# Kernel tuning notes

Hardware: AMD Instinct MI355X
Metric: run time of the kernel (lower is better)

The kernel has to match this reference:

```python
import jax, jax.numpy as jnp
import numpy as np

NUM_HEADS = 16
KERNEL_SIZE = 13  # odd, neighborhood size nh = 6


def setup_inputs() -> dict:
    key = jax.random.key(0)
    ks = jax.random.split(key, 6)
    B, L, C = 4, 4096, 512
    return {
        "x": jax.random.normal(ks[0], (B, L, C), dtype=jnp.float32),
        "qkv_w": jax.random.normal(ks[1], (3 * C, C), dtype=jnp.float32) * (C ** -0.5),
        "qkv_b": jax.random.normal(ks[2], (3 * C,), dtype=jnp.float32) * 0.02,
        "rpb": jax.random.normal(ks[3], (NUM_HEADS, 2 * KERNEL_SIZE - 1), dtype=jnp.float32) * 0.02,
        "proj_w": jax.random.normal(ks[4], (C, C), dtype=jnp.float32) * (C ** -0.5),
        "proj_b": jax.random.normal(ks[5], (C,), dtype=jnp.float32) * 0.02,
    }


def reference(x, qkv_w, qkv_b, rpb, proj_w, proj_b):
    B, L, C = x.shape
    H, K = NUM_HEADS, KERNEL_SIZE
    Dh = C // H
    scale = Dh ** -0.5
    nh = K // 2

    # qkv projection (torch Linear: x @ W.T + b)
    qkv = (x @ qkv_w.T + qkv_b).reshape(B, L, 3, H, Dh)
    qkv = jnp.transpose(qkv, (2, 0, 3, 1, 4))  # (3, B, H, L, Dh)
    q, k, v = qkv[0] * scale, qkv[1], qkv[2]

    # neighborhood indices: window of K keys, shifted (not clipped) at borders
    pos = jnp.arange(L)
    start = jnp.clip(pos - nh, 0, L - K)            # (L,)
    idx = start[:, None] + jnp.arange(K)[None, :]   # (L, K) key positions
    # relative-position-bias index: (key_pos - query_pos) + (K-1), in [0, 2K-2]
    bias_idx = idx - pos[:, None] + (K - 1)         # (L, K)

    k_g = k[:, :, idx, :]                           # (B, H, L, K, Dh)
    attn = jnp.einsum('bhld,bhlkd->bhlk', q, k_g)   # (B, H, L, K)
    attn = attn + rpb[:, bias_idx][None]            # add (H, L, K) bias
    attn = jax.nn.softmax(attn, axis=-1)

    v_g = v[:, :, idx, :]                           # (B, H, L, K, Dh)
    out = jnp.einsum('bhlk,bhlkd->bhld', attn, v_g)  # (B, H, L, Dh)
    out = jnp.transpose(out, (0, 2, 1, 3)).reshape(B, L, C)
    return out @ proj_w.T + proj_b
```

## Files before the change

kernel.cpp:

```cpp
#include <hip/hip_runtime.h>
#include <hip/hip_bf16.h>

#define BATCH   4
#define LSEQ    4096
#define CCH     512
#define HNUM    16
#define DH      32
#define KSZ     13
#define NHALF   6
#define M_TOT   16384
#define N_QKV   1536
#define KDIM    512
#define BK      64

typedef __attribute__((ext_vector_type(8))) short  short8;
typedef __attribute__((ext_vector_type(4))) short  short4_t;
typedef __attribute__((ext_vector_type(4))) float  float4_t;

__device__ __forceinline__ unsigned short f32_to_bf16(float f) {
    union { float f; unsigned int u; } un; un.f = f;
    unsigned int u = un.u;
    u += 0x7FFFu + ((u >> 16) & 1u);
    return (unsigned short)(u >> 16);
}
__device__ __forceinline__ float bf16_to_f32(unsigned short h) {
    union { unsigned int u; float f; } un; un.u = ((unsigned int)h) << 16;
    return un.f;
}

__device__ __forceinline__ void gload_lds16(const unsigned short* g, unsigned short* l) {
    __builtin_amdgcn_global_load_lds(
        (const __attribute__((address_space(1))) unsigned int*)g,
        (__attribute__((address_space(3))) unsigned int*)l,
        16, 0, 0);
}

__global__ void cvt_all(const float4_t* __restrict__ xin,  short4_t* __restrict__ xo,  int nx,
                        const float4_t* __restrict__ w1in, short4_t* __restrict__ w1o, int n1,
                        const float4_t* __restrict__ w2in, short4_t* __restrict__ w2o, int n2) {
    int i = blockIdx.x * blockDim.x + threadIdx.x;
    int stride = gridDim.x * blockDim.x;
    int ntot = nx + n1 + n2;
    for (; i < ntot; i += stride) {
        const float4_t* src; short4_t* dst; int j;
        if (i < nx)            { src = xin;  dst = xo;  j = i; }
        else if (i < nx + n1)  { src = w1in; dst = w1o; j = i - nx; }
        else                   { src = w2in; dst = w2o; j = i - nx - n1; }
        float4_t v = src[j];
        short4_t h;
        h.x = (short)f32_to_bf16(v.x);
        h.y = (short)f32_to_bf16(v.y);
        h.z = (short)f32_to_bf16(v.z);
        h.w = (short)f32_to_bf16(v.w);
        dst[j] = h;
    }
}

__global__ __launch_bounds__(256) void gemm_qkv(
    const unsigned short* __restrict__ Xb,
    const unsigned short* __restrict__ W,
    const float* __restrict__ bias,
    unsigned short* __restrict__ qkvout)
{
    __shared__ __align__(16) unsigned short As[128 * BK];
    __shared__ __align__(16) unsigned short Bs[128 * BK];
    const int tid  = threadIdx.x;
    const int wv   = tid >> 6, ln = tid & 63;

    const int wg   = blockIdx.x;
    const int wgid = (wg & 7) * 192 + (wg >> 3);
    const int m0   = (wgid & 127) * 128;
    const int n0   = (wgid >> 7) * 128;

    const int wm   = (wv >> 1) * 64;
    const int wn   = (wv & 1) * 64;
    const int lr   = ln & 15;
    const int lg   = ln >> 4;
    const int rgrp = ln >> 3;
    const int csw  = ((ln & 7) ^ rgrp) * 8;

    float4_t acc[4][4];
    #pragma unroll
    for (int m = 0; m < 4; ++m)
        #pragma unroll
        for (int n = 0; n < 4; ++n)
            acc[m][n] = (float4_t){0.f, 0.f, 0.f, 0.f};

    for (int k0 = 0; k0 < KDIM; k0 += BK) {
        #pragma unroll
        for (int it = 0; it < 4; ++it) {
            int ch  = it * 4 + wv;
            int row = ch * 8 + rgrp;
            gload_lds16(Xb + (size_t)(m0 + row) * KDIM + k0 + csw,
                        &As[ch * 8 * BK]);
            gload_lds16(W  + (size_t)(n0 + row) * KDIM + k0 + csw,
                        &Bs[ch * 8 * BK]);
        }
        __syncthreads();
        short8 af[2][4], bfr[2][4];
        #pragma unroll
        for (int kk = 0; kk < 2; ++kk) {
            #pragma unroll
            for (int m = 0; m < 4; ++m) {
                int row = wm + m * 16 + lr;
                int c   = (kk * 4 + lg) ^ (row & 7);
                af[kk][m] = *reinterpret_cast<const short8*>(&As[row * BK + c * 8]);
            }
            #pragma unroll
            for (int n = 0; n < 4; ++n) {
                int row = wn + n * 16 + lr;
                int c   = (kk * 4 + lg) ^ (row & 7);
                bfr[kk][n] = *reinterpret_cast<const short8*>(&Bs[row * BK + c * 8]);
            }
        }
        #pragma unroll
        for (int kk = 0; kk < 2; ++kk)
            #pragma unroll
            for (int m = 0; m < 4; ++m)
                #pragma unroll
                for (int n = 0; n < 4; ++n)
                    acc[m][n] = __builtin_amdgcn_mfma_f32_16x16x32_bf16(
                        af[kk][m], bfr[kk][n], acc[m][n], 0, 0, 0);
        __syncthreads();
    }

    const float qscale = 0.17677669529663687f;
    #pragma unroll
    for (int m = 0; m < 4; ++m) {
        #pragma unroll
        for (int n = 0; n < 4; ++n) {
            int gn    = n0 + wn + n * 16 + lr;
            int which = gn >> 9;
            int hh    = (gn >> 5) & 15;
            int dd    = gn & 31;
            float bsv = bias[gn];
            #pragma unroll
            for (int r = 0; r < 4; ++r) {
                int gm = m0 + wm + m * 16 + lg * 4 + r;
                float v = acc[m][n][r] + bsv;
                if (which == 0) v *= qscale;
                int b_ = gm >> 12, l = gm & 4095;
                size_t off = (((size_t)which * BATCH + b_) * HNUM + hh) *
                                 ((size_t)LSEQ * DH) + (size_t)l * DH + dd;
                qkvout[off] = f32_to_bf16(v);
            }
        }
    }
}

__global__ __launch_bounds__(256) void natten_fwd(
    const unsigned short* __restrict__ qkv,
    const float* __restrict__ rpb,
    unsigned short* __restrict__ ctx)
{
    __shared__ __align__(16) unsigned short ks[4 * 268 * 8];
    __shared__ __align__(16) unsigned short vs[4 * 268 * 8];
    __shared__ float rpb_s[2 * KSZ - 1];

    const int t    = threadIdx.x;
    const int lblk = blockIdx.x & 15;
    const int bh   = blockIdx.x >> 4;
    const int hh   = bh & 15, b_ = bh >> 4;
    const int l0   = lblk * 256;

    const int r0    = max(l0 - NHALF, 0);
    const int rend  = min(l0 + 256 + NHALF, LSEQ);
    const int nrows = rend - r0;

    const size_t plane = (size_t)LSEQ * DH;
    const size_t kbase = (((size_t)1 * BATCH + b_) * HNUM + hh) * plane;
    const size_t vbase = (((size_t)2 * BATCH + b_) * HNUM + hh) * plane;

    {
        const int cq  = t >> 6;
        const int rr  = t & 63;
        #pragma unroll
        for (int base = 0; base < 320; base += 64) {
            int row = base + rr;
            if (row < nrows) {
                *reinterpret_cast<short8*>(&ks[(cq * 268 + row) * 8]) =
                    *reinterpret_cast<const short8*>(&qkv[kbase + (size_t)(r0 + row) * DH + cq * 8]);
                *reinterpret_cast<short8*>(&vs[(cq * 268 + row) * 8]) =
                    *reinterpret_cast<const short8*>(&qkv[vbase + (size_t)(r0 + row) * DH + cq * 8]);
            }
        }
    }
    if (t < 2 * KSZ - 1) rpb_s[t] = rpb[hh * (2 * KSZ - 1) + t];
    __syncthreads();

    const int l = l0 + t;
    float q[DH];
    const size_t qoff = (((size_t)0 * BATCH + b_) * HNUM + hh) * plane + (size_t)l * DH;
    #pragma unroll
    for (int cq = 0; cq < 4; ++cq) {
        short8 qv = *reinterpret_cast<const short8*>(&qkv[qoff + cq * 8]);
        #pragma unroll
        for (int e = 0; e < 8; ++e) q[cq * 8 + e] = bf16_to_f32((unsigned short)qv[e]);
    }

    const int start = min(max(l - NHALF, 0), LSEQ - KSZ);
    float logit[KSZ];
    #pragma unroll
    for (int j = 0; j < KSZ; ++j) {
        int kr = start + j - r0;
        float s = 0.f;
        #pragma unroll
        for (int cq = 0; cq < 4; ++cq) {
            short8 kv = *reinterpret_cast<const short8*>(&ks[(cq * 268 + kr) * 8]);
            #pragma unroll
            for (int e = 0; e < 8; ++e)
                s += q[cq * 8 + e] * bf16_to_f32((unsigned short)kv[e]);
        }
        logit[j] = s + rpb_s[start + j - l + (KSZ - 1)];
    }
    float mx = logit[0];
    #pragma unroll
    for (int j = 1; j < KSZ; ++j) mx = fmaxf(mx, logit[j]);
    float p[KSZ], sum = 0.f;
    #pragma unroll
    for (int j = 0; j < KSZ; ++j) { p[j] = __expf(logit[j] - mx); sum += p[j]; }
    const float inv = 1.f / sum;

    float o[DH];
    #pragma unroll
    for (int d = 0; d < DH; ++d) o[d] = 0.f;
    #pragma unroll
    for (int j = 0; j < KSZ; ++j) {
        int kr = start + j - r0;
        float pj = p[j] * inv;
        #pragma unroll
        for (int cq = 0; cq < 4; ++cq) {
            short8 vv = *reinterpret_cast<const short8*>(&vs[(cq * 268 + kr) * 8]);
            #pragma unroll
            for (int e = 0; e < 8; ++e)
                o[cq * 8 + e] += pj * bf16_to_f32((unsigned short)vv[e]);
        }
    }
    const size_t obase = ((size_t)(b_ * LSEQ + l)) * CCH + hh * DH;
    #pragma unroll
    for (int cq = 0; cq < 4; ++cq) {
        short8 ov;
        #pragma unroll
        for (int e = 0; e < 8; ++e) ov[e] = (short)f32_to_bf16(o[cq * 8 + e]);
        *reinterpret_cast<short8*>(&ctx[obase + cq * 8]) = ov;
    }
}

__global__ __launch_bounds__(256) void gemm_proj(
    const unsigned short* __restrict__ Xb,
    const unsigned short* __restrict__ W,
    const float* __restrict__ bias,
    float* __restrict__ out)
{
    __shared__ __align__(16) unsigned short As[128 * BK];
    __shared__ __align__(16) unsigned short Bs[128 * BK];
    const int tid  = threadIdx.x;
    const int wv   = tid >> 6, ln = tid & 63;

    const int wg   = blockIdx.x;
    const int wgid = (wg & 7) * 64 + (wg >> 3);
    const int m0   = (wgid & 127) * 128;
    const int n0   = (wgid >> 7) * 128;

    const int wm   = (wv >> 1) * 64;
    const int wn   = (wv & 1) * 64;
    const int lr   = ln & 15;
    const int lg   = ln >> 4;
    const int rgrp = ln >> 3;
    const int csw  = ((ln & 7) ^ rgrp) * 8;

    float4_t acc[4][4];
    #pragma unroll
    for (int m = 0; m < 4; ++m)
        #pragma unroll
        for (int n = 0; n < 4; ++n)
            acc[m][n] = (float4_t){0.f, 0.f, 0.f, 0.f};

    for (int k0 = 0; k0 < KDIM; k0 += BK) {
        #pragma unroll
        for (int it = 0; it < 4; ++it) {
            int ch  = it * 4 + wv;
            int row = ch * 8 + rgrp;
            gload_lds16(Xb + (size_t)(m0 + row) * KDIM + k0 + csw,
                        &As[ch * 8 * BK]);
            gload_lds16(W  + (size_t)(n0 + row) * KDIM + k0 + csw,
                        &Bs[ch * 8 * BK]);
        }
        __syncthreads();
        short8 af[2][4], bfr[2][4];
        #pragma unroll
        for (int kk = 0; kk < 2; ++kk) {
            #pragma unroll
            for (int m = 0; m < 4; ++m) {
                int row = wm + m * 16 + lr;
                int c   = (kk * 4 + lg) ^ (row & 7);
                af[kk][m] = *reinterpret_cast<const short8*>(&As[row * BK + c * 8]);
            }
            #pragma unroll
            for (int n = 0; n < 4; ++n) {
                int row = wn + n * 16 + lr;
                int c   = (kk * 4 + lg) ^ (row & 7);
                bfr[kk][n] = *reinterpret_cast<const short8*>(&Bs[row * BK + c * 8]);
            }
        }
        #pragma unroll
        for (int kk = 0; kk < 2; ++kk)
            #pragma unroll
            for (int m = 0; m < 4; ++m)
                #pragma unroll
                for (int n = 0; n < 4; ++n)
                    acc[m][n] = __builtin_amdgcn_mfma_f32_16x16x32_bf16(
                        af[kk][m], bfr[kk][n], acc[m][n], 0, 0, 0);
        __syncthreads();
    }

    #pragma unroll
    for (int m = 0; m < 4; ++m) {
        #pragma unroll
        for (int n = 0; n < 4; ++n) {
            int gn = n0 + wn + n * 16 + lr;
            float bsv = bias[gn];
            #pragma unroll
            for (int r = 0; r < 4; ++r) {
                int gm = m0 + wm + m * 16 + lg * 4 + r;
                out[(size_t)gm * CCH + gn] = acc[m][n][r] + bsv;
            }
        }
    }
}

extern "C" void kernel_launch(void* const* d_in, const int* in_sizes, int n_in,
                              void* d_out, int out_size, void* d_ws, size_t ws_size,
                              hipStream_t stream) {
    const float* x      = (const float*)d_in[0];
    const float* qkv_w  = (const float*)d_in[1];
    const float* qkv_b  = (const float*)d_in[2];
    const float* rpb    = (const float*)d_in[3];
    const float* proj_w = (const float*)d_in[4];
    const float* proj_b = (const float*)d_in[5];
    float* out = (float*)d_out;
    char* ws = (char*)d_ws;

    unsigned short* qkv = (unsigned short*)(ws);
    unsigned short* xb  = (unsigned short*)(ws + 50331648);
    unsigned short* ctx = (unsigned short*)(ws + 50331648);
    unsigned short* wq  = (unsigned short*)(ws + 67108864);
    unsigned short* wp  = (unsigned short*)(ws + 68681728);

    cvt_all<<<2048, 256, 0, stream>>>(
        (const float4_t*)x,      (short4_t*)xb, M_TOT * KDIM / 4,
        (const float4_t*)qkv_w,  (short4_t*)wq, 786432 / 4,
        (const float4_t*)proj_w, (short4_t*)wp, 262144 / 4);

    gemm_qkv<<<1536, 256, 0, stream>>>(xb, wq, qkv_b, qkv);

    natten_fwd<<<BATCH * HNUM * (LSEQ / 256), 256, 0, stream>>>(qkv, rpb, ctx);

    gemm_proj<<<512, 256, 0, stream>>>(ctx, wp, proj_b, out);
}
```

Measured before the change: 93.70 us.

## Double-buffer LDS tiles in QKV and projection GEMMs with async prefetch

Both GEMM kernels now use dynamic shared memory with two A/B buffers, so the next K-tile is loaded while the current one feeds MFMAs. The wait uses an explicit vmcnt and raw barriers in place of __syncthreads. The XCD-aware block swizzle is replaced by a plain 2D grid, which changes L2 locality across chiplets. LDS per block doubles to 64KB, which may reduce occupancy.

```diff
diff --git a/kernel.cpp b/kernel.cpp
--- a/kernel.cpp
+++ b/kernel.cpp
@@ -62,16 +62,11 @@
     const float* __restrict__ bias,
     unsigned short* __restrict__ qkvout)
 {
-    __shared__ __align__(16) unsigned short As[128 * BK];
-    __shared__ __align__(16) unsigned short Bs[128 * BK];
+    extern __shared__ __align__(16) unsigned short lds[];
     const int tid  = threadIdx.x;
     const int wv   = tid >> 6, ln = tid & 63;
-
-    const int wg   = blockIdx.x;
-    const int wgid = (wg & 7) * 192 + (wg >> 3);
-    const int m0   = (wgid & 127) * 128;
-    const int n0   = (wgid >> 7) * 128;
-
+    const int m0   = blockIdx.x * 128;
+    const int n0   = blockIdx.y * 128;
     const int wm   = (wv >> 1) * 64;
     const int wn   = (wv & 1) * 64;
     const int lr   = ln & 15;
@@ -86,17 +81,32 @@
         for (int n = 0; n < 4; ++n)
             acc[m][n] = (float4_t){0.f, 0.f, 0.f, 0.f};
 
-    for (int k0 = 0; k0 < KDIM; k0 += BK) {
-        #pragma unroll
-        for (int it = 0; it < 4; ++it) {
-            int ch  = it * 4 + wv;
-            int row = ch * 8 + rgrp;
-            gload_lds16(Xb + (size_t)(m0 + row) * KDIM + k0 + csw,
-                        &As[ch * 8 * BK]);
-            gload_lds16(W  + (size_t)(n0 + row) * KDIM + k0 + csw,
-                        &Bs[ch * 8 * BK]);
-        }
-        __syncthreads();
+    #define STAGE(k0_, abuf_, bbuf_) do {                                     \
+        _Pragma("unroll")                                                     \
+        for (int it_ = 0; it_ < 4; ++it_) {                                   \
+            int ch_  = it_ * 4 + wv;                 \
+            int row_ = ch_ * 8 + rgrp;                                        \
+            gload_lds16(Xb + (size_t)(m0 + row_) * KDIM + (k0_) + csw,        \
+                        (abuf_) + ch_ * 8 * BK);                              \
+            gload_lds16(W  + (size_t)(n0 + row_) * KDIM + (k0_) + csw,        \
+                        (bbuf_) + ch_ * 8 * BK);                              \
+        }                                                                     \
+    } while (0)
+
+    unsigned short* Ac = lds;           unsigned short* Bc = lds + 8192;
+    unsigned short* An = lds + 16384;   unsigned short* Bn = lds + 24576;
+
+    STAGE(0, Ac, Bc);
+
+    for (int t = 0; t < 8; ++t) {
+        if (t < 7) {
+            STAGE((t + 1) * BK, An, Bn);
+            asm volatile("s_waitcnt vmcnt(8)" ::: "memory");
+        } else {
+            asm volatile("s_waitcnt vmcnt(0)" ::: "memory");
+        }
+        __builtin_amdgcn_s_barrier();
+
         short8 af[2][4], bfr[2][4];
         #pragma unroll
         for (int kk = 0; kk < 2; ++kk) {
@@ -104,13 +114,13 @@
             for (int m = 0; m < 4; ++m) {
                 int row = wm + m * 16 + lr;
                 int c   = (kk * 4 + lg) ^ (row & 7);
-                af[kk][m] = *reinterpret_cast<const short8*>(&As[row * BK + c * 8]);
+                af[kk][m] = *reinterpret_cast<const short8*>(&Ac[row * BK + c * 8]);
             }
             #pragma unroll
             for (int n = 0; n < 4; ++n) {
                 int row = wn + n * 16 + lr;
                 int c   = (kk * 4 + lg) ^ (row & 7);
-                bfr[kk][n] = *reinterpret_cast<const short8*>(&Bs[row * BK + c * 8]);
+                bfr[kk][n] = *reinterpret_cast<const short8*>(&Bc[row * BK + c * 8]);
             }
         }
         #pragma unroll
@@ -121,8 +131,12 @@
                 for (int n = 0; n < 4; ++n)
                     acc[m][n] = __builtin_amdgcn_mfma_f32_16x16x32_bf16(
                         af[kk][m], bfr[kk][n], acc[m][n], 0, 0, 0);
-        __syncthreads();
-    }
+
+        if (t < 7) __builtin_amdgcn_s_barrier();
+        unsigned short* tA = Ac; Ac = An; An = tA;
+        unsigned short* tB = Bc; Bc = Bn; Bn = tB;
+    }
+    #undef STAGE
 
     const float qscale = 0.17677669529663687f;
     #pragma unroll
@@ -252,16 +266,11 @@
     const float* __restrict__ bias,
     float* __restrict__ out)
 {
-    __shared__ __align__(16) unsigned short As[128 * BK];
-    __shared__ __align__(16) unsigned short Bs[128 * BK];
+    extern __shared__ __align__(16) unsigned short lds[];
     const int tid  = threadIdx.x;
     const int wv   = tid >> 6, ln = tid & 63;
-
-    const int wg   = blockIdx.x;
-    const int wgid = (wg & 7) * 64 + (wg >> 3);
-    const int m0   = (wgid & 127) * 128;
-    const int n0   = (wgid >> 7) * 128;
-
+    const int m0   = blockIdx.x * 128;
+    const int n0   = blockIdx.y * 128;
     const int wm   = (wv >> 1) * 64;
     const int wn   = (wv & 1) * 64;
     const int lr   = ln & 15;
@@ -276,17 +285,32 @@
         for (int n = 0; n < 4; ++n)
             acc[m][n] = (float4_t){0.f, 0.f, 0.f, 0.f};
 
-    for (int k0 = 0; k0 < KDIM; k0 += BK) {
-        #pragma unroll
-        for (int it = 0; it < 4; ++it) {
-            int ch  = it * 4 + wv;
-            int row = ch * 8 + rgrp;
-            gload_lds16(Xb + (size_t)(m0 + row) * KDIM + k0 + csw,
-                        &As[ch * 8 * BK]);
-            gload_lds16(W  + (size_t)(n0 + row) * KDIM + k0 + csw,
-                        &Bs[ch * 8 * BK]);
-        }
-        __syncthreads();
+    #define STAGEP(k0_, abuf_, bbuf_) do {                                    \
+        _Pragma("unroll")                                                     \
+        for (int it_ = 0; it_ < 4; ++it_) {                                   \
+            int ch_  = it_ * 4 + wv;                                          \
+            int row_ = ch_ * 8 + rgrp;                                        \
+            gload_lds16(Xb + (size_t)(m0 + row_) * KDIM + (k0_) + csw,        \
+                        (abuf_) + ch_ * 8 * BK);                              \
+            gload_lds16(W  + (size_t)(n0 + row_) * KDIM + (k0_) + csw,        \
+                        (bbuf_) + ch_ * 8 * BK);                              \
+        }                                                                     \
+    } while (0)
+
+    unsigned short* Ac = lds;           unsigned short* Bc = lds + 8192;
+    unsigned short* An = lds + 16384;   unsigned short* Bn = lds + 24576;
+
+    STAGEP(0, Ac, Bc);
+
+    for (int t = 0; t < 8; ++t) {
+        if (t < 7) {
+            STAGEP((t + 1) * BK, An, Bn);
+            asm volatile("s_waitcnt vmcnt(8)" ::: "memory");
+        } else {
+            asm volatile("s_waitcnt vmcnt(0)" ::: "memory");
+        }
+        __builtin_amdgcn_s_barrier();
+
         short8 af[2][4], bfr[2][4];
         #pragma unroll
         for (int kk = 0; kk < 2; ++kk) {
@@ -294,13 +318,13 @@
             for (int m = 0; m < 4; ++m) {
                 int row = wm + m * 16 + lr;
                 int c   = (kk * 4 + lg) ^ (row & 7);
-                af[kk][m] = *reinterpret_cast<const short8*>(&As[row * BK + c * 8]);
+                af[kk][m] = *reinterpret_cast<const short8*>(&Ac[row * BK + c * 8]);
             }
             #pragma unroll
             for (int n = 0; n < 4; ++n) {
                 int row = wn + n * 16 + lr;
                 int c   = (kk * 4 + lg) ^ (row & 7);
-                bfr[kk][n] = *reinterpret_cast<const short8*>(&Bs[row * BK + c * 8]);
+                bfr[kk][n] = *reinterpret_cast<const short8*>(&Bc[row * BK + c * 8]);
             }
         }
         #pragma unroll
@@ -311,8 +335,12 @@
                 for (int n = 0; n < 4; ++n)
                     acc[m][n] = __builtin_amdgcn_mfma_f32_16x16x32_bf16(
                         af[kk][m], bfr[kk][n], acc[m][n], 0, 0, 0);
-        __syncthreads();
-    }
+
+        if (t < 7) __builtin_amdgcn_s_barrier();
+        unsigned short* tA = Ac; Ac = An; An = tA;
+        unsigned short* tB = Bc; Bc = Bn; Bn = tB;
+    }
+    #undef STAGEP
 
     #pragma unroll
     for (int m = 0; m < 4; ++m) {
@@ -352,9 +380,11 @@
         (const float4_t*)qkv_w,  (short4_t*)wq, 786432 / 4,
         (const float4_t*)proj_w, (short4_t*)wp, 262144 / 4);
 
-    gemm_qkv<<<1536, 256, 0, stream>>>(xb, wq, qkv_b, qkv);
+    dim3 g1(M_TOT / 128, N_QKV / 128);
+    gemm_qkv<<<g1, 256, 65536, stream>>>(xb, wq, qkv_b, qkv);
 
     natten_fwd<<<BATCH * HNUM * (LSEQ / 256), 256, 0, stream>>>(qkv, rpb, ctx);
 
-    gemm_proj<<<512, 256, 0, stream>>>(ctx, wp, proj_b, out);
-}
+    dim3 g2(M_TOT / 128, CCH / 128);
+    gemm_proj<<<g2, 256, 65536, stream>>>(ctx, wp, proj_b, out);
+}
```

Result: faster. 79.42 us (-15.2%).
